# Kernel optimization log

Hardware: AMD Instinct MI355X
Metric: run time of the kernel (lower is better)

The kernel has to match this reference:

```python
import jax, jax.numpy as jnp
import numpy as np

NUM_EMB = 512
LATENT = 128
TEXT_DIM = 512


def setup_inputs() -> dict:
    key = jax.random.key(0)
    ks = jax.random.split(key, 12)
    B, N = 64, 8192
    x = jax.random.normal(ks[0], (B, N, 3), dtype=jnp.float32)
    s = jax.random.normal(ks[1], (B, N), dtype=jnp.float32)
    e = jax.random.normal(ks[2], (B, TEXT_DIM), dtype=jnp.float32)
    # point_mlp: Linear(4,64) -> ReLU -> Linear(64,128); weights stored (in,out)
    W1 = jax.random.normal(ks[3], (4, 64), dtype=jnp.float32) * 0.5
    b1 = jnp.zeros((64,), dtype=jnp.float32)
    W2 = jax.random.normal(ks[4], (64, 128), dtype=jnp.float32) * 0.125
    b2 = jnp.zeros((128,), dtype=jnp.float32)
    # latent_mlp: Linear(128+512,256) -> ReLU -> Linear(256,128)
    W3 = jax.random.normal(ks[5], (128 + TEXT_DIM, 256), dtype=jnp.float32) * 0.04
    b3 = jnp.zeros((256,), dtype=jnp.float32)
    W4 = jax.random.normal(ks[6], (256, LATENT), dtype=jnp.float32) * 0.0625
    b4 = jnp.zeros((LATENT,), dtype=jnp.float32)
    # codebook init uniform(-1/K, 1/K) as in torch code
    codebook = jax.random.uniform(ks[7], (NUM_EMB, LATENT), dtype=jnp.float32,
                                  minval=-1.0 / NUM_EMB, maxval=1.0 / NUM_EMB)
    return {"x": x, "s": s, "e": e, "W1": W1, "b1": b1, "W2": W2, "b2": b2,
            "W3": W3, "b3": b3, "W4": W4, "b4": b4, "codebook": codebook}


def reference(x, s, e, W1, b1, W2, b2, W3, b3, W4, b4, codebook):
    # PointNet feature extraction
    point_inp = jnp.concatenate([x, s[..., None]], axis=-1)        # (B,N,4)
    h = jax.nn.relu(point_inp @ W1 + b1)                           # (B,N,64)
    point_feat = h @ W2 + b2                                       # (B,N,128)
    global_feat = jnp.max(point_feat, axis=1)                      # (B,128)
    combined = jnp.concatenate([global_feat, e], axis=-1)          # (B,640)
    z_e = jax.nn.relu(combined @ W3 + b3) @ W4 + b4                # (B,latent)
    # VQ: squared-L2 distances to codebook, argmin, gather
    dists = (jnp.sum(z_e * z_e, axis=1, keepdims=True)
             - 2.0 * (z_e @ codebook.T)
             + jnp.sum(codebook * codebook, axis=1))               # (B,K)
    indices = jnp.argmin(dists, axis=1)                            # (B,)
    z_q = codebook[indices]                                        # (B,latent)
    sg = jax.lax.stop_gradient
    codebook_loss = jnp.mean((z_q - sg(z_e)) ** 2)
    commitment_loss = jnp.mean((z_e - sg(z_q)) ** 2)
    z_q_st = z_e + sg(z_q - z_e)
    return (z_q_st, z_e, codebook_loss, commitment_loss, indices)
```

## Files before the change

### kernel.cpp

```cpp
#include <hip/hip_runtime.h>

typedef unsigned int u32;
typedef __attribute__((ext_vector_type(4))) unsigned int u32x4;
typedef __attribute__((ext_vector_type(8))) short s16x8;
typedef __attribute__((ext_vector_type(4))) float f32x4;

__device__ __forceinline__ u32 rne_hi(float a) {
    u32 u = __float_as_uint(a);
    return (u + 0x7FFFu + ((u >> 16) & 1u)) & 0xFFFF0000u;
}

__global__ __launch_bounds__(256, 4) void k1_pointfeat(
    const float* __restrict__ x, const float* __restrict__ s,
    const float* __restrict__ W1, const float* __restrict__ b1,
    const float* __restrict__ W2, float* __restrict__ ws_part)
{
    __shared__ __align__(16) u32 Hlds[2 * 2 * 64 * 36];
    const int tid   = threadIdx.x;
    const int lane  = tid & 63;
    const int point = tid & 63;
    const int kq    = __builtin_amdgcn_readfirstlane(tid >> 6);
    const int rl    = lane & 15;
    const int kg2   = lane >> 4;

    const int p0 = blockIdx.x * 512;

    s16x8 wbh[2][2], wbl[2][2];
    #pragma unroll
    for (int n = 0; n < 2; ++n)
        #pragma unroll
        for (int sl2 = 0; sl2 < 2; ++sl2)
            #pragma unroll
            for (int j = 0; j < 8; ++j) {
                float f = W2[(size_t)(kg2 * 8 + j + sl2 * 32) * 128 + kq * 32 + n * 16 + rl];
                u32 hb = rne_hi(f);
                float lo = f - __uint_as_float(hb);
                u32 lb = rne_hi(lo);
                wbh[n][sl2][j] = (short)(hb >> 16);
                wbl[n][sl2][j] = (short)(lb >> 16);
            }

    float rmax0 = -3.402823466e38f, rmax1 = -3.402823466e38f;

#define STAGE_GROUP(GG, PX, PY, PZ, PW)                                        \
    {                                                                          \
        u32* Hw = &Hlds[((GG) & 1) * 4608 + point * 36 + kq * 8];              \
        _Pragma("unroll")                                                      \
        for (int h = 0; h < 2; ++h) {                                          \
            u32 hp[4], lp[4];                                                  \
            _Pragma("unroll")                                                  \
            for (int c = 0; c < 4; ++c) {                                      \
                const int k0 = kq * 16 + h * 8 + c * 2;                        \
                float a0 = fmaf(PX, W1[k0],                                    \
                           fmaf(PY, W1[64 + k0],                               \
                           fmaf(PZ, W1[128 + k0],                              \
                           fmaf(PW, W1[192 + k0], b1[k0]))));                  \
                float a1 = fmaf(PX, W1[k0 + 1],                                \
                           fmaf(PY, W1[65 + k0],                               \
                           fmaf(PZ, W1[129 + k0],                              \
                           fmaf(PW, W1[193 + k0], b1[k0 + 1]))));              \
                a0 = a0 > 0.f ? a0 : 0.f;                                      \
                a1 = a1 > 0.f ? a1 : 0.f;                                      \
                u32 h0 = rne_hi(a0), h1 = rne_hi(a1);                          \
                float l0 = a0 - __uint_as_float(h0);                           \
                float l1 = a1 - __uint_as_float(h1);                           \
                hp[c] = __builtin_amdgcn_perm(h1, h0, 0x07060302u);            \
                lp[c] = __builtin_amdgcn_perm(__float_as_uint(l1),             \
                                              __float_as_uint(l0), 0x07060302u);\
            }                                                                  \
            u32x4 vh = {hp[0], hp[1], hp[2], hp[3]};                           \
            u32x4 vl = {lp[0], lp[1], lp[2], lp[3]};                           \
            *(u32x4*)(Hw + h * 4)        = vh;                                 \
            *(u32x4*)(Hw + 2304 + h * 4) = vl;                                 \
        }                                                                      \
    }

    {
        const int gp = p0 + point;
        float px = x[(size_t)gp * 3 + 0], py = x[(size_t)gp * 3 + 1];
        float pz = x[(size_t)gp * 3 + 2], pw = s[gp];
        STAGE_GROUP(0, px, py, pz, pw)
    }
    float pxn, pyn, pzn, pwn;
    {
        const int gp = p0 + 64 + point;
        pxn = x[(size_t)gp * 3 + 0]; pyn = x[(size_t)gp * 3 + 1];
        pzn = x[(size_t)gp * 3 + 2]; pwn = s[gp];
    }

    #pragma unroll 1
    for (int g = 0; g < 8; ++g) {
        __syncthreads();
        const u32* Hb = &Hlds[(g & 1) * 4608];
        f32x4 acc[4][2] = {};
        __builtin_amdgcn_s_setprio(1);
        #pragma unroll
        for (int sl2 = 0; sl2 < 2; ++sl2) {
            s16x8 ah[4], al[4];
            #pragma unroll
            for (int m = 0; m < 4; ++m) {
                const u32* base = Hb + (m * 16 + rl) * 36 + sl2 * 16 + kg2 * 4;
                ah[m] = *(const s16x8*)(base);
                al[m] = *(const s16x8*)(base + 2304);
            }
            #pragma unroll
            for (int m = 0; m < 4; ++m)
                #pragma unroll
                for (int n = 0; n < 2; ++n)
                    acc[m][n] = __builtin_amdgcn_mfma_f32_16x16x32_bf16(
                        ah[m], wbh[n][sl2], acc[m][n], 0, 0, 0);
            #pragma unroll
            for (int m = 0; m < 4; ++m)
                #pragma unroll
                for (int n = 0; n < 2; ++n)
                    acc[m][n] = __builtin_amdgcn_mfma_f32_16x16x32_bf16(
                        ah[m], wbl[n][sl2], acc[m][n], 0, 0, 0);
            #pragma unroll
            for (int m = 0; m < 4; ++m)
                #pragma unroll
                for (int n = 0; n < 2; ++n)
                    acc[m][n] = __builtin_amdgcn_mfma_f32_16x16x32_bf16(
                        al[m], wbh[n][sl2], acc[m][n], 0, 0, 0);
        }
        __builtin_amdgcn_s_setprio(0);
        if (g < 7) {
            STAGE_GROUP(g + 1, pxn, pyn, pzn, pwn)
            if (g < 6) {
                const int gp = p0 + (g + 2) * 64 + point;
                pxn = x[(size_t)gp * 3 + 0]; pyn = x[(size_t)gp * 3 + 1];
                pzn = x[(size_t)gp * 3 + 2]; pwn = s[gp];
            }
        }
        #pragma unroll
        for (int m = 0; m < 4; ++m)
            #pragma unroll
            for (int r = 0; r < 4; ++r) {
                rmax0 = fmaxf(rmax0, acc[m][0][r]);
                rmax1 = fmaxf(rmax1, acc[m][1][r]);
            }
    }
#undef STAGE_GROUP

    rmax0 = fmaxf(rmax0, __shfl_xor(rmax0, 16, 64));
    rmax0 = fmaxf(rmax0, __shfl_xor(rmax0, 32, 64));
    rmax1 = fmaxf(rmax1, __shfl_xor(rmax1, 16, 64));
    rmax1 = fmaxf(rmax1, __shfl_xor(rmax1, 32, 64));
    if (lane < 16) {
        ws_part[blockIdx.x * 128 + kq * 32 + lane]      = rmax0;
        ws_part[blockIdx.x * 128 + kq * 32 + 16 + lane] = rmax1;
    }
}

__global__ __launch_bounds__(256) void k2a_hidden(
    const float* __restrict__ ws_part, const float* __restrict__ b2,
    const float* __restrict__ e,
    const float* __restrict__ W3, const float* __restrict__ b3,
    float* __restrict__ ws_hid)
{
    const int blk = blockIdx.x;
    const int b   = blk >> 2;
    const int c   = blk & 3;
    const int tid = threadIdx.x;
    const int u   = tid & 63;
    const int part = tid >> 6;
    __shared__ float comb[640];
    __shared__ float psum[4][64];

    for (int i = tid; i < 640; i += 256) {
        float v;
        if (i < 128) {
            const float* __restrict__ pp = ws_part + (size_t)b * 16 * 128 + i;
            float m = pp[0];
            #pragma unroll
            for (int t = 1; t < 16; ++t) m = fmaxf(m, pp[t * 128]);
            v = m + b2[i];
        } else {
            v = e[b * 512 + (i - 128)];
        }
        comb[i] = v;
    }
    __syncthreads();

    const int gu = c * 64 + u;
    const float* __restrict__ Wp = W3 + (size_t)(part * 160) * 256 + gu;
    const float* __restrict__ cp = comb + part * 160;
    float a = 0.f;
    for (int i = 0; i < 160; ++i) a = fmaf(cp[i], Wp[(size_t)i * 256], a);
    psum[part][u] = a;
    __syncthreads();
    if (tid < 64) {
        float hv = psum[0][u] + psum[1][u] + psum[2][u] + psum[3][u] + b3[gu];
        ws_hid[b * 256 + gu] = hv > 0.f ? hv : 0.f;
    }
}

__global__ __launch_bounds__(512) void k2b_vq(
    const float* __restrict__ ws_hid,
    const float* __restrict__ W4, const float* __restrict__ b4,
    const float* __restrict__ cb, float* __restrict__ out,
    float* __restrict__ ws_loss)
{
    const int b = blockIdx.x, tid = threadIdx.x;
    __shared__ float hid[256];
    __shared__ float psum[4][128];
    __shared__ float ze[128];
    __shared__ float red_d[512];
    __shared__ int   red_i[512];
    __shared__ float lred[128];
    __shared__ float zzs;

    if (tid < 256) hid[tid] = ws_hid[b * 256 + tid];
    __syncthreads();

    {
        const int u = tid & 127, part = tid >> 7;
        const float* __restrict__ Wp = W4 + (size_t)(part * 64) * 128 + u;
        const float* __restrict__ hp = hid + part * 64;
        float a = 0.f;
        for (int i = 0; i < 64; ++i) a = fmaf(hp[i], Wp[(size_t)i * 128], a);
        psum[part][u] = a;
    }
    __syncthreads();
    if (tid < 128) {
        float a = psum[0][tid] + psum[1][tid] + psum[2][tid] + psum[3][tid] + b4[tid];
        ze[tid] = a;
        out[8192 + b * 128 + tid] = a;
    }
    __syncthreads();

    if (tid < 64) {
        float t = ze[tid] * ze[tid] + ze[tid + 64] * ze[tid + 64];
        #pragma unroll
        for (int d = 1; d < 64; d <<= 1) t += __shfl_xor(t, d, 64);
        if (tid == 0) zzs = t;
    }
    __syncthreads();

    {
        float dot = 0.f, cc = 0.f;
        const f32x4* __restrict__ cp = (const f32x4*)(cb + (size_t)tid * 128);
        for (int k4 = 0; k4 < 32; ++k4) {
            f32x4 v = cp[k4];
            dot = fmaf(ze[k4 * 4 + 0], v.x, dot);
            cc  = fmaf(v.x, v.x, cc);
            dot = fmaf(ze[k4 * 4 + 1], v.y, dot);
            cc  = fmaf(v.y, v.y, cc);
            dot = fmaf(ze[k4 * 4 + 2], v.z, dot);
            cc  = fmaf(v.z, v.z, cc);
            dot = fmaf(ze[k4 * 4 + 3], v.w, dot);
            cc  = fmaf(v.w, v.w, cc);
        }
        red_d[tid] = zzs - 2.f * dot + cc;
        red_i[tid] = tid;
    }
    __syncthreads();

    for (int sft = 256; sft >= 1; sft >>= 1) {
        if (tid < sft) {
            float da = red_d[tid], db = red_d[tid + sft];
            int   ia = red_i[tid], ib = red_i[tid + sft];
            if (db < da || (db == da && ib < ia)) { red_d[tid] = db; red_i[tid] = ib; }
        }
        __syncthreads();
    }
    const int bc = red_i[0];

    if (tid < 128) {
        float zq  = cb[(size_t)bc * 128 + tid];
        float zev = ze[tid];
        out[b * 128 + tid] = zev + (zq - zev);
        float d = zq - zev;
        lred[tid] = d * d;
    }
    if (tid == 0) out[16386 + b] = (float)bc;
    __syncthreads();
    if (tid < 64) {
        float t = lred[tid] + lred[tid + 64];
        #pragma unroll
        for (int d = 1; d < 64; d <<= 1) t += __shfl_xor(t, d, 64);
        if (tid == 0) ws_loss[b] = t;
    }
}

__global__ void k3_loss(const float* __restrict__ ws_loss, float* __restrict__ out)
{
    const int t = threadIdx.x;
    float v = ws_loss[t];
    #pragma unroll
    for (int d = 1; d < 64; d <<= 1) v += __shfl_xor(v, d, 64);
    if (t == 0) {
        float m = v / 8192.f;
        out[16384] = m;
        out[16385] = m;
    }
}

extern "C" void kernel_launch(void* const* d_in, const int* in_sizes, int n_in,
                              void* d_out, int out_size, void* d_ws, size_t ws_size,
                              hipStream_t stream) {
    const float* x  = (const float*)d_in[0];
    const float* s  = (const float*)d_in[1];
    const float* e  = (const float*)d_in[2];
    const float* W1 = (const float*)d_in[3];
    const float* b1 = (const float*)d_in[4];
    const float* W2 = (const float*)d_in[5];
    const float* b2 = (const float*)d_in[6];
    const float* W3 = (const float*)d_in[7];
    const float* b3 = (const float*)d_in[8];
    const float* W4 = (const float*)d_in[9];
    const float* b4 = (const float*)d_in[10];
    const float* cb = (const float*)d_in[11];
    float* out = (float*)d_out;

    float* ws_part = (float*)d_ws;
    float* ws_hid  = (float*)d_ws + 1024 * 128;
    float* ws_loss = (float*)d_ws + 1024 * 128 + 64 * 256;

    k1_pointfeat<<<1024, 256, 0, stream>>>(x, s, W1, b1, W2, ws_part);
    k2a_hidden<<<256, 256, 0, stream>>>(ws_part, b2, e, W3, b3, ws_hid);
    k2b_vq<<<64, 512, 0, stream>>>(ws_hid, W4, b4, cb, out, ws_loss);
    k3_loss<<<1, 64, 0, stream>>>(ws_loss, out);
}
```

Baseline: 47.42 us.

## Restructure point-feature kernel to 2 waves per block with 64-column tiles

```diff
diff --git a/kernel.cpp b/kernel.cpp
--- a/kernel.cpp
+++ b/kernel.cpp
@@ -1,4 +1,5 @@
 #include <hip/hip_runtime.h>
+#include <hip/hip_bf16.h>
 
 typedef unsigned int u32;
 typedef __attribute__((ext_vector_type(4))) unsigned int u32x4;
@@ -9,30 +10,35 @@
     u32 u = __float_as_uint(a);
     return (u + 0x7FFFu + ((u >> 16) & 1u)) & 0xFFFF0000u;
 }
-
-__global__ __launch_bounds__(256, 4) void k1_pointfeat(
+__device__ __forceinline__ u32 pk_bf16(float a0, float a1) {
+    __hip_bfloat162 pk2 = __float22bfloat162_rn(make_float2(a0, a1));
+    u32 r;
+    __builtin_memcpy(&r, &pk2, 4);
+    return r;
+}
+
+__global__ __launch_bounds__(128, 2) void k1_pointfeat(
     const float* __restrict__ x, const float* __restrict__ s,
     const float* __restrict__ W1, const float* __restrict__ b1,
     const float* __restrict__ W2, float* __restrict__ ws_part)
 {
-    __shared__ __align__(16) u32 Hlds[2 * 2 * 64 * 36];
-    const int tid   = threadIdx.x;
-    const int lane  = tid & 63;
-    const int point = tid & 63;
-    const int kq    = __builtin_amdgcn_readfirstlane(tid >> 6);
-    const int rl    = lane & 15;
-    const int kg2   = lane >> 4;
+    __shared__ __align__(16) u32 Hlds[2 * 2 * 32 * 36];
+    const int tid  = threadIdx.x;
+    const int lane = tid & 63;
+    const int w    = __builtin_amdgcn_readfirstlane(tid >> 6);
+    const int rl   = lane & 15;
+    const int kg2  = lane >> 4;
 
     const int p0 = blockIdx.x * 512;
 
-    s16x8 wbh[2][2], wbl[2][2];
+    s16x8 wbh[4][2], wbl[4][2];
     #pragma unroll
-    for (int n = 0; n < 2; ++n)
+    for (int n = 0; n < 4; ++n)
         #pragma unroll
         for (int sl2 = 0; sl2 < 2; ++sl2)
             #pragma unroll
             for (int j = 0; j < 8; ++j) {
-                float f = W2[(size_t)(kg2 * 8 + j + sl2 * 32) * 128 + kq * 32 + n * 16 + rl];
+                float f = W2[(size_t)(kg2 * 8 + j + sl2 * 32) * 128 + w * 64 + n * 16 + rl];
                 u32 hb = rne_hi(f);
                 float lo = f - __uint_as_float(hb);
                 u32 lb = rne_hi(lo);
@@ -40,17 +46,18 @@
                 wbl[n][sl2][j] = (short)(lb >> 16);
             }
 
-    float rmax0 = -3.402823466e38f, rmax1 = -3.402823466e38f;
+    float rmaxn[4] = {-3.402823466e38f, -3.402823466e38f,
+                      -3.402823466e38f, -3.402823466e38f};
 
 #define STAGE_GROUP(GG, PX, PY, PZ, PW)                                        \
     {                                                                          \
-        u32* Hw = &Hlds[((GG) & 1) * 4608 + point * 36 + kq * 8];              \
+        u32* Hw = &Hlds[((GG) & 1) * 2304 + (w * 16 + rl) * 36 + kg2 * 8];     \
         _Pragma("unroll")                                                      \
         for (int h = 0; h < 2; ++h) {                                          \
             u32 hp[4], lp[4];                                                  \
             _Pragma("unroll")                                                  \
             for (int c = 0; c < 4; ++c) {                                      \
-                const int k0 = kq * 16 + h * 8 + c * 2;                        \
+                const int k0 = kg2 * 16 + h * 8 + c * 2;                       \
                 float a0 = fmaf(PX, W1[k0],                                    \
                            fmaf(PY, W1[64 + k0],                               \
                            fmaf(PZ, W1[128 + k0],                              \
@@ -61,93 +68,93 @@
                            fmaf(PW, W1[193 + k0], b1[k0 + 1]))));              \
                 a0 = a0 > 0.f ? a0 : 0.f;                                      \
                 a1 = a1 > 0.f ? a1 : 0.f;                                      \
-                u32 h0 = rne_hi(a0), h1 = rne_hi(a1);                          \
-                float l0 = a0 - __uint_as_float(h0);                           \
-                float l1 = a1 - __uint_as_float(h1);                           \
-                hp[c] = __builtin_amdgcn_perm(h1, h0, 0x07060302u);            \
-                lp[c] = __builtin_amdgcn_perm(__float_as_uint(l1),             \
-                                              __float_as_uint(l0), 0x07060302u);\
+                u32 ph = pk_bf16(a0, a1);                                      \
+                float h0 = __uint_as_float(ph << 16);                          \
+                float h1 = __uint_as_float(ph & 0xFFFF0000u);                  \
+                u32 pl = pk_bf16(a0 - h0, a1 - h1);                            \
+                hp[c] = ph;                                                    \
+                lp[c] = pl;                                                    \
             }                                                                  \
             u32x4 vh = {hp[0], hp[1], hp[2], hp[3]};                           \
             u32x4 vl = {lp[0], lp[1], lp[2], lp[3]};                           \
             *(u32x4*)(Hw + h * 4)        = vh;                                 \
-            *(u32x4*)(Hw + 2304 + h * 4) = vl;                                 \
+            *(u32x4*)(Hw + 1152 + h * 4) = vl;                                 \
         }                                                                      \
     }
 
     {
-        const int gp = p0 + point;
+        const int gp = p0 + w * 16 + rl;
         float px = x[(size_t)gp * 3 + 0], py = x[(size_t)gp * 3 + 1];
         float pz = x[(size_t)gp * 3 + 2], pw = s[gp];
         STAGE_GROUP(0, px, py, pz, pw)
     }
     float pxn, pyn, pzn, pwn;
     {
-        const int gp = p0 + 64 + point;
+        const int gp = p0 + 32 + w * 16 + rl;
         pxn = x[(size_t)gp * 3 + 0]; pyn = x[(size_t)gp * 3 + 1];
         pzn = x[(size_t)gp * 3 + 2]; pwn = s[gp];
     }
 
     #pragma unroll 1
-    for (int g = 0; g < 8; ++g) {
+    for (int g = 0; g < 16; ++g) {
         __syncthreads();
-        const u32* Hb = &Hlds[(g & 1) * 4608];
-        f32x4 acc[4][2] = {};
-        __builtin_amdgcn_s_setprio(1);
+        const u32* Hb = &Hlds[(g & 1) * 2304];
+        f32x4 acc[2][4] = {};
         #pragma unroll
         for (int sl2 = 0; sl2 < 2; ++sl2) {
-            s16x8 ah[4], al[4];
-            #pragma unroll
-            for (int m = 0; m < 4; ++m) {
+            s16x8 ah[2], al[2];
+            #pragma unroll
+            for (int m = 0; m < 2; ++m) {
                 const u32* base = Hb + (m * 16 + rl) * 36 + sl2 * 16 + kg2 * 4;
                 ah[m] = *(const s16x8*)(base);
-                al[m] = *(const s16x8*)(base + 2304);
+                al[m] = *(const s16x8*)(base + 1152);
             }
             #pragma unroll
-            for (int m = 0; m < 4; ++m)
+            for (int m = 0; m < 2; ++m)
                 #pragma unroll
-                for (int n = 0; n < 2; ++n)
+                for (int n = 0; n < 4; ++n)
                     acc[m][n] = __builtin_amdgcn_mfma_f32_16x16x32_bf16(
                         ah[m], wbh[n][sl2], acc[m][n], 0, 0, 0);
             #pragma unroll
-            for (int m = 0; m < 4; ++m)
+            for (int m = 0; m < 2; ++m)
                 #pragma unroll
-                for (int n = 0; n < 2; ++n)
+                for (int n = 0; n < 4; ++n)
                     acc[m][n] = __builtin_amdgcn_mfma_f32_16x16x32_bf16(
                         ah[m], wbl[n][sl2], acc[m][n], 0, 0, 0);
             #pragma unroll
-            for (int m = 0; m < 4; ++m)
+            for (int m = 0; m < 2; ++m)
                 #pragma unroll
-                for (int n = 0; n < 2; ++n)
+                for (int n = 0; n < 4; ++n)
                     acc[m][n] = __builtin_amdgcn_mfma_f32_16x16x32_bf16(
                         al[m], wbh[n][sl2], acc[m][n], 0, 0, 0);
         }
-        __builtin_amdgcn_s_setprio(0);
-        if (g < 7) {
+        if (g < 15) {
             STAGE_GROUP(g + 1, pxn, pyn, pzn, pwn)
-            if (g < 6) {
-                const int gp = p0 + (g + 2) * 64 + point;
+            if (g < 14) {
+                const int gp = p0 + (g + 2) * 32 + w * 16 + rl;
                 pxn = x[(size_t)gp * 3 + 0]; pyn = x[(size_t)gp * 3 + 1];
                 pzn = x[(size_t)gp * 3 + 2]; pwn = s[gp];
             }
         }
         #pragma unroll
-        for (int m = 0; m < 4; ++m)
-            #pragma unroll
-            for (int r = 0; r < 4; ++r) {
-                rmax0 = fmaxf(rmax0, acc[m][0][r]);
-                rmax1 = fmaxf(rmax1, acc[m][1][r]);
-            }
+        for (int m = 0; m < 2; ++m)
+            #pragma unroll
+            for (int n = 0; n < 4; ++n)
+                #pragma unroll
+                for (int r = 0; r < 4; ++r)
+                    rmaxn[n] = fmaxf(rmaxn[n], acc[m][n][r]);
     }
 #undef STAGE_GROUP
 
-    rmax0 = fmaxf(rmax0, __shfl_xor(rmax0, 16, 64));
-    rmax0 = fmaxf(rmax0, __shfl_xor(rmax0, 32, 64));
-    rmax1 = fmaxf(rmax1, __shfl_xor(rmax1, 16, 64));
-    rmax1 = fmaxf(rmax1, __shfl_xor(rmax1, 32, 64));
+    #pragma unroll
+    for (int n = 0; n < 4; ++n) {
+        rmaxn[n] = fmaxf(rmaxn[n], __shfl_xor(rmaxn[n], 16, 64));
+        rmaxn[n] = fmaxf(rmaxn[n], __shfl_xor(rmaxn[n], 32, 64));
+    }
     if (lane < 16) {
-        ws_part[blockIdx.x * 128 + kq * 32 + lane]      = rmax0;
-        ws_part[blockIdx.x * 128 + kq * 32 + 16 + lane] = rmax1;
+        #pragma unroll
+        for (int n = 0; n < 4; ++n)
+            ws_part[blockIdx.x * 128 + w * 64 + n * 16 + lane] = rmaxn[n];
     }
 }
 
@@ -316,7 +323,7 @@
     float* ws_hid  = (float*)d_ws + 1024 * 128;
     float* ws_loss = (float*)d_ws + 1024 * 128 + 64 * 256;
 
-    k1_pointfeat<<<1024, 256, 0, stream>>>(x, s, W1, b1, W2, ws_part);
+    k1_pointfeat<<<1024, 128, 0, stream>>>(x, s, W1, b1, W2, ws_part);
     k2a_hidden<<<256, 256, 0, stream>>>(ws_part, b2, e, W3, b3, ws_hid);
     k2b_vq<<<64, 512, 0, stream>>>(ws_hid, W4, b4, cb, out, ws_loss);
     k3_loss<<<1, 64, 0, stream>>>(ws_loss, out);
```

New measurement: 57.20 us. 20.6% more time.

## Interleave next-group layer-1 compute with MFMA chain and use hardware bf16 packing

Applied to the files above, without the earlier changes.

```diff
diff --git a/kernel.cpp b/kernel.cpp
--- a/kernel.cpp
+++ b/kernel.cpp
@@ -1,4 +1,5 @@
 #include <hip/hip_runtime.h>
+#include <hip/hip_bf16.h>
 
 typedef unsigned int u32;
 typedef __attribute__((ext_vector_type(4))) unsigned int u32x4;
@@ -9,8 +10,14 @@
     u32 u = __float_as_uint(a);
     return (u + 0x7FFFu + ((u >> 16) & 1u)) & 0xFFFF0000u;
 }
-
-__global__ __launch_bounds__(256, 4) void k1_pointfeat(
+__device__ __forceinline__ u32 pk_bf16(float a0, float a1) {
+    __hip_bfloat162 pk2 = __float22bfloat162_rn(make_float2(a0, a1));
+    u32 r;
+    __builtin_memcpy(&r, &pk2, 4);
+    return r;
+}
+
+__global__ __launch_bounds__(256) void k1_pointfeat(
     const float* __restrict__ x, const float* __restrict__ s,
     const float* __restrict__ W1, const float* __restrict__ b1,
     const float* __restrict__ W2, float* __restrict__ ws_part)
@@ -42,9 +49,8 @@
 
     float rmax0 = -3.402823466e38f, rmax1 = -3.402823466e38f;
 
-#define STAGE_GROUP(GG, PX, PY, PZ, PW)                                        \
+#define STAGE_COMPUTE(PX, PY, PZ, PW, VH0, VH1, VL0, VL1)                      \
     {                                                                          \
-        u32* Hw = &Hlds[((GG) & 1) * 4608 + point * 36 + kq * 8];              \
         _Pragma("unroll")                                                      \
         for (int h = 0; h < 2; ++h) {                                          \
             u32 hp[4], lp[4];                                                  \
@@ -61,25 +67,34 @@
                            fmaf(PW, W1[193 + k0], b1[k0 + 1]))));              \
                 a0 = a0 > 0.f ? a0 : 0.f;                                      \
                 a1 = a1 > 0.f ? a1 : 0.f;                                      \
-                u32 h0 = rne_hi(a0), h1 = rne_hi(a1);                          \
-                float l0 = a0 - __uint_as_float(h0);                           \
-                float l1 = a1 - __uint_as_float(h1);                           \
-                hp[c] = __builtin_amdgcn_perm(h1, h0, 0x07060302u);            \
-                lp[c] = __builtin_amdgcn_perm(__float_as_uint(l1),             \
-                                              __float_as_uint(l0), 0x07060302u);\
+                u32 ph = pk_bf16(a0, a1);                                      \
+                float h0 = __uint_as_float(ph << 16);                          \
+                float h1 = __uint_as_float(ph & 0xFFFF0000u);                  \
+                u32 pl = pk_bf16(a0 - h0, a1 - h1);                            \
+                hp[c] = ph; lp[c] = pl;                                        \
             }                                                                  \
-            u32x4 vh = {hp[0], hp[1], hp[2], hp[3]};                           \
-            u32x4 vl = {lp[0], lp[1], lp[2], lp[3]};                           \
-            *(u32x4*)(Hw + h * 4)        = vh;                                 \
-            *(u32x4*)(Hw + 2304 + h * 4) = vl;                                 \
+            if (h == 0) { VH0 = (u32x4){hp[0],hp[1],hp[2],hp[3]};              \
+                          VL0 = (u32x4){lp[0],lp[1],lp[2],lp[3]}; }            \
+            else        { VH1 = (u32x4){hp[0],hp[1],hp[2],hp[3]};              \
+                          VL1 = (u32x4){lp[0],lp[1],lp[2],lp[3]}; }            \
         }                                                                      \
+    }
+#define STAGE_WRITE(GG, VH0, VH1, VL0, VL1)                                    \
+    {                                                                          \
+        u32* Hw = &Hlds[((GG) & 1) * 4608 + point * 36 + kq * 8];              \
+        *(u32x4*)(Hw)            = VH0;                                        \
+        *(u32x4*)(Hw + 4)        = VH1;                                        \
+        *(u32x4*)(Hw + 2304)     = VL0;                                        \
+        *(u32x4*)(Hw + 2304 + 4) = VL1;                                        \
     }
 
     {
         const int gp = p0 + point;
         float px = x[(size_t)gp * 3 + 0], py = x[(size_t)gp * 3 + 1];
         float pz = x[(size_t)gp * 3 + 2], pw = s[gp];
-        STAGE_GROUP(0, px, py, pz, pw)
+        u32x4 vh0, vh1, vl0, vl1;
+        STAGE_COMPUTE(px, py, pz, pw, vh0, vh1, vl0, vl1)
+        STAGE_WRITE(0, vh0, vh1, vl0, vl1)
     }
     float pxn, pyn, pzn, pwn;
     {
@@ -92,45 +107,76 @@
     for (int g = 0; g < 8; ++g) {
         __syncthreads();
         const u32* Hb = &Hlds[(g & 1) * 4608];
+
+        s16x8 ah0[4], al0[4];
+        #pragma unroll
+        for (int m = 0; m < 4; ++m) {
+            const u32* base = Hb + (m * 16 + rl) * 36 + kg2 * 4;
+            ah0[m] = *(const s16x8*)(base);
+            al0[m] = *(const s16x8*)(base + 2304);
+        }
+
+        u32x4 vh0, vh1, vl0, vl1;
+        if (g < 7) {
+            STAGE_COMPUTE(pxn, pyn, pzn, pwn, vh0, vh1, vl0, vl1)
+        }
+
         f32x4 acc[4][2] = {};
-        __builtin_amdgcn_s_setprio(1);
-        #pragma unroll
-        for (int sl2 = 0; sl2 < 2; ++sl2) {
-            s16x8 ah[4], al[4];
-            #pragma unroll
-            for (int m = 0; m < 4; ++m) {
-                const u32* base = Hb + (m * 16 + rl) * 36 + sl2 * 16 + kg2 * 4;
-                ah[m] = *(const s16x8*)(base);
-                al[m] = *(const s16x8*)(base + 2304);
-            }
-            #pragma unroll
-            for (int m = 0; m < 4; ++m)
-                #pragma unroll
-                for (int n = 0; n < 2; ++n)
-                    acc[m][n] = __builtin_amdgcn_mfma_f32_16x16x32_bf16(
-                        ah[m], wbh[n][sl2], acc[m][n], 0, 0, 0);
-            #pragma unroll
-            for (int m = 0; m < 4; ++m)
-                #pragma unroll
-                for (int n = 0; n < 2; ++n)
-                    acc[m][n] = __builtin_amdgcn_mfma_f32_16x16x32_bf16(
-                        ah[m], wbl[n][sl2], acc[m][n], 0, 0, 0);
-            #pragma unroll
-            for (int m = 0; m < 4; ++m)
-                #pragma unroll
-                for (int n = 0; n < 2; ++n)
-                    acc[m][n] = __builtin_amdgcn_mfma_f32_16x16x32_bf16(
-                        al[m], wbh[n][sl2], acc[m][n], 0, 0, 0);
-        }
-        __builtin_amdgcn_s_setprio(0);
+        #pragma unroll
+        for (int m = 0; m < 4; ++m)
+            #pragma unroll
+            for (int n = 0; n < 2; ++n)
+                acc[m][n] = __builtin_amdgcn_mfma_f32_16x16x32_bf16(
+                    ah0[m], wbh[n][0], acc[m][n], 0, 0, 0);
+        #pragma unroll
+        for (int m = 0; m < 4; ++m)
+            #pragma unroll
+            for (int n = 0; n < 2; ++n)
+                acc[m][n] = __builtin_amdgcn_mfma_f32_16x16x32_bf16(
+                    ah0[m], wbl[n][0], acc[m][n], 0, 0, 0);
+        #pragma unroll
+        for (int m = 0; m < 4; ++m)
+            #pragma unroll
+            for (int n = 0; n < 2; ++n)
+                acc[m][n] = __builtin_amdgcn_mfma_f32_16x16x32_bf16(
+                    al0[m], wbh[n][0], acc[m][n], 0, 0, 0);
+
+        s16x8 ah1[4], al1[4];
+        #pragma unroll
+        for (int m = 0; m < 4; ++m) {
+            const u32* base = Hb + (m * 16 + rl) * 36 + 16 + kg2 * 4;
+            ah1[m] = *(const s16x8*)(base);
+            al1[m] = *(const s16x8*)(base + 2304);
+        }
+        if (g < 6) {
+            const int gp = p0 + (g + 2) * 64 + point;
+            pxn = x[(size_t)gp * 3 + 0]; pyn = x[(size_t)gp * 3 + 1];
+            pzn = x[(size_t)gp * 3 + 2]; pwn = s[gp];
+        }
+
+        #pragma unroll
+        for (int m = 0; m < 4; ++m)
+            #pragma unroll
+            for (int n = 0; n < 2; ++n)
+                acc[m][n] = __builtin_amdgcn_mfma_f32_16x16x32_bf16(
+                    ah1[m], wbh[n][1], acc[m][n], 0, 0, 0);
+        #pragma unroll
+        for (int m = 0; m < 4; ++m)
+            #pragma unroll
+            for (int n = 0; n < 2; ++n)
+                acc[m][n] = __builtin_amdgcn_mfma_f32_16x16x32_bf16(
+                    ah1[m], wbl[n][1], acc[m][n], 0, 0, 0);
+        #pragma unroll
+        for (int m = 0; m < 4; ++m)
+            #pragma unroll
+            for (int n = 0; n < 2; ++n)
+                acc[m][n] = __builtin_amdgcn_mfma_f32_16x16x32_bf16(
+                    al1[m], wbh[n][1], acc[m][n], 0, 0, 0);
+
         if (g < 7) {
-            STAGE_GROUP(g + 1, pxn, pyn, pzn, pwn)
-            if (g < 6) {
-                const int gp = p0 + (g + 2) * 64 + point;
-                pxn = x[(size_t)gp * 3 + 0]; pyn = x[(size_t)gp * 3 + 1];
-                pzn = x[(size_t)gp * 3 + 2]; pwn = s[gp];
-            }
-        }
+            STAGE_WRITE(g + 1, vh0, vh1, vl0, vl1)
+        }
+
         #pragma unroll
         for (int m = 0; m < 4; ++m)
             #pragma unroll
@@ -139,7 +185,8 @@
                 rmax1 = fmaxf(rmax1, acc[m][1][r]);
             }
     }
-#undef STAGE_GROUP
+#undef STAGE_COMPUTE
+#undef STAGE_WRITE
 
     rmax0 = fmaxf(rmax0, __shfl_xor(rmax0, 16, 64));
     rmax0 = fmaxf(rmax0, __shfl_xor(rmax0, 32, 64));
```

New measurement: 49.36 us. 4.1% more time.
